# Kernel optimization log

Measured on AMD Instinct MI355X. Metric: run time of the kernel, lower is better.

The kernel has to match this reference:

```python
import jax, jax.numpy as jnp
import numpy as np

# DeepNovo config constants
MASS_H2O = 18.01056
MASS_NH3 = 17.02655
MS_RESOLUTION = 10.0          # bins per Dalton
WINDOW_SIZE = 10
MAX_MZ = 30000                # 3000 Da * 10 bins/Da
_PAD, _GO, _EOS = 0, 1, 2
VOCAB = 26
BATCH = 32768


def setup_inputs() -> dict:
    key = jax.random.key(0)
    k1, k2, k3, k4 = jax.random.split(key, 4)
    spectrum = jax.random.uniform(k1, (MAX_MZ,), dtype=jnp.float32)
    pepmass = jax.random.uniform(k2, (BATCH,), dtype=jnp.float32, minval=500.0, maxval=2500.0)
    prefix_mass = jax.random.uniform(k3, (BATCH,), dtype=jnp.float32) * pepmass * 0.8
    # amino-acid residue masses roughly in [57, 186] Da
    masses = jax.random.uniform(k4, (VOCAB,), dtype=jnp.float32, minval=57.0, maxval=186.0)
    return {"spectrum": spectrum, "pepmass": pepmass, "prefix_mass": prefix_mass,
            "masses": masses, "direction": 0}


def reference(spectrum, pepmass, prefix_mass, masses, direction):
    if direction == 0:
        first_label, last_label = _GO, _EOS
        cb = prefix_mass[:, None] + masses[None, :]      # [B, V]
        cy = pepmass[:, None] - cb
    else:
        first_label, last_label = _EOS, _GO
        cy = prefix_mass[:, None] + masses[None, :]
        cb = pepmass[:, None] - cy
    # 8 ion types: b, b-H2O, b-NH3, b++, y, y-H2O, y-NH3, y++  -> [B, V, 8]
    ion_mass = jnp.stack([cb, cb - MASS_H2O, cb - MASS_NH3, cb / 2,
                          cy, cy - MASS_H2O, cy - MASS_NH3, cy / 2], axis=-1)
    inf_idx = jnp.round(ion_mass * MS_RESOLUTION).astype(jnp.int32) - WINDOW_SIZE // 2
    valid = (inf_idx >= 0) & (inf_idx <= MAX_MZ - WINDOW_SIZE)   # [B, V, 8]
    safe = jnp.where(valid, inf_idx, 0)
    slices = safe[..., None] + jnp.arange(WINDOW_SIZE, dtype=jnp.int32)  # [B, V, 8, W]
    gathered = jnp.take(spectrum, slices) * valid[..., None].astype(spectrum.dtype)
    # zero out FIRST/LAST/PAD vocab rows (for both directions the set is {_PAD,_GO,_EOS})
    label_mask = jnp.ones((VOCAB,), spectrum.dtype).at[
        jnp.array([_PAD, first_label, last_label])].set(0.0)
    return gathered * label_mask[None, :, None, None]
```

## Files before the change

kernel.cpp:

```cpp
#include <hip/hip_runtime.h>
#include <hip/hip_fp16.h>


#define MASS_H2O 18.01056f
#define MASS_NH3 17.02655f

typedef float floatx4 __attribute__((ext_vector_type(4)));

constexpr int MAX_MZ = 30000;
constexpr int WIN = 10;
constexpr int CPR = 520;
constexpr int BLOCK = 960;
constexpr int GRID  = 494;
constexpr int THREADS = GRID * BLOCK;
constexpr int ROW_STEP = THREADS / CPR;

__global__ __launch_bounds__(BLOCK, 8) void intensity_kernel(
    const float* __restrict__ spectrum,
    const float* __restrict__ pepmass,
    const float* __restrict__ prefix_mass,
    const float* __restrict__ masses,
    const int*   __restrict__ dir_p,
    float* __restrict__ out,
    int batch)
{
    __shared__ __half sspec[MAX_MZ];

    {
        const float2* sp2 = reinterpret_cast<const float2*>(spectrum);
        __half2* dst = reinterpret_cast<__half2*>(sspec);
        for (int i = threadIdx.x; i < MAX_MZ / 2; i += BLOCK) {
            float2 t = sp2[i];
            dst[i] = __floats2half2_rn(t.x, t.y);
        }
    }

    const int tid = (int)blockIdx.x * BLOCK + (int)threadIdx.x;

    const int col  = tid % CPR;
    const int row0 = tid / CPR;
    const int v = col / 20;
    const int q = col - v * 20;
    const float ms = masses[v];
    const float lm = (v > 2) ? 1.0f : 0.0f;
    const int dir = dir_p[0];

    bool  su[4];
    float aj[4];
    float mj10[4];
    int   wj[4];
#pragma unroll
    for (int j = 0; j < 4; ++j) {
        int e   = 4 * q + j;
        int ion = e / 10;
        wj[j] = e - ion * 10;
        bool scy = (ion >= 4);
        su[j] = scy ^ (dir != 0);
        int kk = ion & 3;
        aj[j]   = (kk == 1) ? -MASS_H2O : (kk == 2) ? -MASS_NH3 : 0.0f;
        mj10[j] = (kk == 3) ? 5.0f : 10.0f;
    }

    __syncthreads();

    const int n = (batch - row0 + ROW_STEP - 1) / ROW_STEP;
    floatx4* op = reinterpret_cast<floatx4*>(out) + tid;

    int row = row0;
#pragma unroll 2
    for (int k = 0; k < n; ++k, row += ROW_STEP) {
        float pm = pepmass[row];
        float pf = prefix_mass[row];
        float t = pf + ms;
        float u = pm - t;

        float vals[4];
#pragma unroll
        for (int j = 0; j < 4; ++j) {
            float base = su[j] ? u : t;
            float f = (base + aj[j]) * mj10[j];
            int idx = (int)rintf(f) - (WIN / 2);
            bool valid = (unsigned)idx <= (unsigned)(MAX_MZ - WIN);
            int safe = valid ? idx : 0;
            float s = __half2float(sspec[safe + wj[j]]);
            vals[j] = valid ? s * lm : 0.0f;
        }

        floatx4 r;
        r.x = vals[0]; r.y = vals[1]; r.z = vals[2]; r.w = vals[3];
        op[(size_t)k * (size_t)THREADS] = r;
    }
}

extern "C" void kernel_launch(void* const* d_in, const int* in_sizes, int n_in,
                              void* d_out, int out_size, void* d_ws, size_t ws_size,
                              hipStream_t stream) {
    const float* spectrum    = (const float*)d_in[0];
    const float* pepmass     = (const float*)d_in[1];
    const float* prefix_mass = (const float*)d_in[2];
    const float* masses      = (const float*)d_in[3];
    const int*   direction   = (const int*)d_in[4];
    float* out = (float*)d_out;

    int batch = in_sizes[1];
    intensity_kernel<<<GRID, BLOCK, 0, stream>>>(
        spectrum, pepmass, prefix_mass, masses, direction, out, batch);
}
```

Measured before the change: 274.2 us.

## Stage per-row masses in LDS and fetch spectrum pairs with dword loads

```diff
diff --git a/kernel.cpp b/kernel.cpp
--- a/kernel.cpp
+++ b/kernel.cpp
@@ -14,6 +14,9 @@
 constexpr int GRID  = 494;
 constexpr int THREADS = GRID * BLOCK;
 constexpr int ROW_STEP = THREADS / CPR;
+constexpr int KMAX = 37;
+constexpr int DROWS = 3;
+constexpr int SPAD = 30004;
 
 __global__ __launch_bounds__(BLOCK, 8) void intensity_kernel(
     const float* __restrict__ spectrum,
@@ -24,70 +27,98 @@
     float* __restrict__ out,
     int batch)
 {
-    __shared__ __half sspec[MAX_MZ];
+    __shared__ __half  sspec[SPAD];
+    __shared__ float2  spmf[DROWS * KMAX];
+
+    const int tid  = (int)blockIdx.x * BLOCK + (int)threadIdx.x;
+    const int blkR = ((int)blockIdx.x * BLOCK) / CPR;
 
     {
         const float2* sp2 = reinterpret_cast<const float2*>(spectrum);
         __half2* dst = reinterpret_cast<__half2*>(sspec);
+#pragma unroll 4
         for (int i = threadIdx.x; i < MAX_MZ / 2; i += BLOCK) {
             float2 t = sp2[i];
             dst[i] = __floats2half2_rn(t.x, t.y);
         }
+        if (threadIdx.x < (SPAD - MAX_MZ) / 2)
+            dst[MAX_MZ / 2 + threadIdx.x] = __floats2half2_rn(0.f, 0.f);
     }
-
-    const int tid = (int)blockIdx.x * BLOCK + (int)threadIdx.x;
+    {
+        int i = threadIdx.x;
+        if (i < DROWS * KMAX) {
+            int d = i / KMAX;
+            int k = i - d * KMAX;
+            int r = blkR + d + k * ROW_STEP;
+            float2 val = {0.0f, 0.0f};
+            if (r < batch) { val.x = pepmass[r]; val.y = prefix_mass[r]; }
+            spmf[i] = val;
+        }
+    }
 
     const int col  = tid % CPR;
     const int row0 = tid / CPR;
+    const int doff = (row0 - blkR) * KMAX;
     const int v = col / 20;
     const int q = col - v * 20;
     const float ms = masses[v];
-    const float lm = (v > 2) ? 1.0f : 0.0f;
+    const bool lmb = (v > 2);
     const int dir = dir_p[0];
 
-    bool  su[4];
-    float aj[4];
-    float mj10[4];
-    int   wj[4];
-#pragma unroll
-    for (int j = 0; j < 4; ++j) {
-        int e   = 4 * q + j;
-        int ion = e / 10;
-        wj[j] = e - ion * 10;
-        bool scy = (ion >= 4);
-        su[j] = scy ^ (dir != 0);
-        int kk = ion & 3;
-        aj[j]   = (kk == 1) ? -MASS_H2O : (kk == 2) ? -MASS_NH3 : 0.0f;
-        mj10[j] = (kk == 3) ? 5.0f : 10.0f;
-    }
+    const int e0 = 4 * q;
+    const int ionA = e0 / 10;
+    const int wp0  = e0 - ionA * 10;
+    const int ionB = (e0 + 2) / 10;
+    const int wp1  = (e0 + 2) - ionB * 10;
+
+    const bool  suA = ((ionA >= 4) ^ (dir != 0));
+    const bool  suB = ((ionB >= 4) ^ (dir != 0));
+    const int   kA = ionA & 3, kB = ionB & 3;
+    const float ajA = (kA == 1) ? -MASS_H2O : (kA == 2) ? -MASS_NH3 : 0.0f;
+    const float ajB = (kB == 1) ? -MASS_H2O : (kB == 2) ? -MASS_NH3 : 0.0f;
+    const float mjA = (kA == 3) ? 5.0f : 10.0f;
+    const float mjB = (kB == 3) ? 5.0f : 10.0f;
 
     __syncthreads();
 
     const int n = (batch - row0 + ROW_STEP - 1) / ROW_STEP;
     floatx4* op = reinterpret_cast<floatx4*>(out) + tid;
+    const uint32_t* spec32 = reinterpret_cast<const uint32_t*>(sspec);
 
-    int row = row0;
 #pragma unroll 2
-    for (int k = 0; k < n; ++k, row += ROW_STEP) {
-        float pm = pepmass[row];
-        float pf = prefix_mass[row];
-        float t = pf + ms;
-        float u = pm - t;
+    for (int k = 0; k < n; ++k) {
+        float2 pp = spmf[doff + k];
+        float t = pp.y + ms;
+        float u = pp.x - t;
 
-        float vals[4];
-#pragma unroll
-        for (int j = 0; j < 4; ++j) {
-            float base = su[j] ? u : t;
-            float f = (base + aj[j]) * mj10[j];
-            int idx = (int)rintf(f) - (WIN / 2);
-            bool valid = (unsigned)idx <= (unsigned)(MAX_MZ - WIN);
-            int safe = valid ? idx : 0;
-            float s = __half2float(sspec[safe + wj[j]]);
-            vals[j] = valid ? s * lm : 0.0f;
-        }
+        float baseA = suA ? u : t;
+        float fA = (baseA + ajA) * mjA;
+        int   idxA = (int)rintf(fA) - (WIN / 2);
+        bool  vA = (unsigned)idxA <= (unsigned)(MAX_MZ - WIN);
+        int   safeA = vA ? idxA : 0;
+        float okA = (vA && lmb) ? 1.0f : 0.0f;
+        float baseB = suB ? u : t;
+        float fB = (baseB + ajB) * mjB;
+        int   idxB = (int)rintf(fB) - (WIN / 2);
+        bool  vB = (unsigned)idxB <= (unsigned)(MAX_MZ - WIN);
+        int   safeB = vB ? idxB : 0;
+        float okB = (vB && lmb) ? 1.0f : 0.0f;
+
+        int h0 = safeA + wp0;
+        int h1 = safeB + wp1;
+        int dw0 = h0 >> 1, dw1 = h1 >> 1;
+        uint32_t a0 = spec32[dw0], a1 = spec32[dw0 + 1];
+        uint32_t b0 = spec32[dw1], b1 = spec32[dw1 + 1];
+        uint32_t r0 = (uint32_t)(((((uint64_t)a1) << 32) | a0) >> ((h0 & 1) << 4));
+        uint32_t r1 = (uint32_t)(((((uint64_t)b1) << 32) | b0) >> ((h1 & 1) << 4));
+        __half2 hv0 = *reinterpret_cast<__half2*>(&r0);
+        __half2 hv1 = *reinterpret_cast<__half2*>(&r1);
 
         floatx4 r;
-        r.x = vals[0]; r.y = vals[1]; r.z = vals[2]; r.w = vals[3];
+        r.x = __low2float(hv0)  * okA;
+        r.y = __high2float(hv0) * okA;
+        r.z = __low2float(hv1)  * okB;
+        r.w = __high2float(hv1) * okB;
         op[(size_t)k * (size_t)THREADS] = r;
     }
 }
```

New measurement: 273.5 us. Within noise of the previous version (-0.2%).
